# Kernel optimization log

Measured on AMD Instinct MI355X. Metric: run time of the kernel, lower is better.

## Reference

```python
import jax, jax.numpy as jnp
import numpy as np

N_NODES = 10000
N_EDGES = 320000
IN_DIM = 128
HID = 256


def setup_inputs() -> dict:
    key = jax.random.key(0)
    ks = jax.random.split(key, 10)
    s_in = 1.0 / np.sqrt(IN_DIM)
    s_h = 1.0 / np.sqrt(HID)
    return {
        "x": jax.random.normal(ks[0], (N_NODES, IN_DIM), dtype=jnp.float32),
        "edge_index": jax.random.randint(ks[1], (2, N_EDGES), 0, N_NODES, dtype=jnp.int64),
        # feature_projector Linear(IN_DIM -> HID)
        "Wp": jax.random.uniform(ks[2], (IN_DIM, HID), jnp.float32, -s_in, s_in),
        "bp": jax.random.uniform(ks[3], (HID,), jnp.float32, -s_in, s_in),
        # LSTM(input=HID, hidden=HID) params, torch layout [4H, H], gate order i,f,g,o
        "W_ih": jax.random.uniform(ks[4], (4 * HID, HID), jnp.float32, -s_h, s_h),
        "W_hh": jax.random.uniform(ks[5], (4 * HID, HID), jnp.float32, -s_h, s_h),
        "b_ih": jax.random.uniform(ks[6], (4 * HID,), jnp.float32, -s_h, s_h),
        "b_hh": jax.random.uniform(ks[7], (4 * HID,), jnp.float32, -s_h, s_h),
        # EvolveGCN-O initial weight [H, H] (glorot-style)
        "initial_weight": jax.random.normal(ks[8], (HID, HID), dtype=jnp.float32) * np.sqrt(2.0 / (2 * HID)),
        # GCNConv bias
        "b_gcn": jnp.zeros((HID,), dtype=jnp.float32),
    }


def _forward(x, edge_index, Wp, bp, W_ih, W_hh, b_ih, b_hh, initial_weight, b_gcn):
    n = x.shape[0]
    # 1) feature projection
    h = x @ Wp + bp  # [N, H]
    # 2) EvolveGCN-O: one LSTM step on the weight matrix (rows = batch),
    #    with h0 = c0 = initial_weight; evolved hidden state is the GCN weight.
    gates = initial_weight @ W_ih.T + b_ih + initial_weight @ W_hh.T + b_hh  # [H, 4H]
    i_g, f_g, g_g, o_g = jnp.split(gates, 4, axis=-1)
    c = jax.nn.sigmoid(f_g) * initial_weight + jax.nn.sigmoid(i_g) * jnp.tanh(g_g)
    W = jax.nn.sigmoid(o_g) * jnp.tanh(c)  # [H, H]
    # 3) GCN propagation with fixed W: out = D^{-1/2}(A+I)D^{-1/2} (h W) + b
    hw = h @ W  # [N, H]
    self_loop = jnp.arange(n, dtype=edge_index.dtype)
    src = jnp.concatenate([edge_index[0], self_loop])
    dst = jnp.concatenate([edge_index[1], self_loop])
    ones = jnp.ones(src.shape[0], dtype=hw.dtype)
    deg = jax.ops.segment_sum(ones, dst, num_segments=n)  # in-degree incl. self loop
    dinv = jnp.where(deg > 0, jax.lax.rsqrt(deg), 0.0)
    norm = dinv[src] * dinv[dst]  # [E+N]
    out = jax.ops.segment_sum(hw[src] * norm[:, None], dst, num_segments=n)
    return out + b_gcn


def reference(x, edge_index, Wp, bp, W_ih, W_hh, b_ih, b_hh, initial_weight, b_gcn):
    return _forward(x, edge_index, Wp, bp, W_ih, W_hh, b_ih, b_hh, initial_weight, b_gcn)
```

## Files before the change

kernel.cpp:

```cpp
#include <hip/hip_runtime.h>
#include <math.h>

#define N_NODES 10000
#define N_EDGES 320000
#define IN_DIM  128
#define HID     256
#define CAP     128

#define NB_GATES 64
#define NB_FILL  313
#define NB_XCVT  80


__device__ __forceinline__ unsigned bf16rne(float f) {
    union { float f; unsigned u; } c; c.f = f;
    return (c.u + 0x7FFFu + ((c.u >> 16) & 1u)) >> 16;
}

__global__ __launch_bounds__(256)
void k_prep(const int* __restrict__ ei, int* __restrict__ cursor,
            int* __restrict__ bucket, const float* __restrict__ iw,
            const float* __restrict__ wih, const float* __restrict__ whh,
            float* __restrict__ G, const float* __restrict__ x,
            unsigned* __restrict__ xb) {
    __shared__ float smem[8192];
    if (blockIdx.x >= NB_GATES + NB_FILL) {
        int tid = (blockIdx.x - NB_GATES - NB_FILL) * 256 + threadIdx.x;
        const float2* x2 = (const float2*)x;
        #pragma unroll
        for (int it = 0; it < 32; ++it) {
            int idx = tid + it * (NB_XCVT * 256);
            if (idx < N_NODES * 64) {
                float2 v = x2[idx];
                xb[idx] = bf16rne(v.x) | (bf16rne(v.y) << 16);
            }
        }
        return;
    }
    if (blockIdx.x >= NB_GATES) {
        int e = ((blockIdx.x - NB_GATES) * 256 + threadIdx.x) * 4;
        if (e + 3 < N_EDGES) {
            int4 s4 = *(const int4*)&ei[e];
            int4 d4 = *(const int4*)&ei[N_EDGES + e];
            int p0 = atomicAdd(&cursor[d4.x], 1);
            if (p0 < CAP) bucket[d4.x * CAP + p0] = s4.x;
            int p1 = atomicAdd(&cursor[d4.y], 1);
            if (p1 < CAP) bucket[d4.y * CAP + p1] = s4.y;
            int p2 = atomicAdd(&cursor[d4.z], 1);
            if (p2 < CAP) bucket[d4.z * CAP + p2] = s4.z;
            int p3 = atomicAdd(&cursor[d4.w], 1);
            if (p3 < CAP) bucket[d4.w * CAP + p3] = s4.w;
        } else {
            for (int q = e; q < N_EDGES; ++q) {
                int s = ei[q];
                int d = ei[N_EDGES + q];
                int pos = atomicAdd(&cursor[d], 1);
                if (pos < CAP) bucket[d * CAP + pos] = s;
            }
        }
        return;
    }
    int bid = blockIdx.x;
    int m0 = (bid & 3) * 64, n0 = (bid >> 2) * 64;
    float (*aT)[64] = (float(*)[64])smem;
    float (*bS)[64] = (float(*)[64])(smem + 4096);
    int t = threadIdx.x;
    int tm = t & 15, tn = t >> 4;
    float acc[4][4] = {};
    for (int kt = 0; kt < 4; ++kt) {
        int k0 = kt * 64;
        int row = t >> 2;
        #pragma unroll
        for (int r = 0; r < 4; ++r) {
            int k4 = 4 * (t & 3) + r;
            float4 av = *(const float4*)&iw[(m0 + row) * HID + k0 + 4 * k4];
            aT[4 * k4 + 0][row] = av.x; aT[4 * k4 + 1][row] = av.y;
            aT[4 * k4 + 2][row] = av.z; aT[4 * k4 + 3][row] = av.w;
            float4 b1 = *(const float4*)&wih[(n0 + row) * HID + k0 + 4 * k4];
            float4 b2 = *(const float4*)&whh[(n0 + row) * HID + k0 + 4 * k4];
            bS[4 * k4 + 0][row] = b1.x + b2.x; bS[4 * k4 + 1][row] = b1.y + b2.y;
            bS[4 * k4 + 2][row] = b1.z + b2.z; bS[4 * k4 + 3][row] = b1.w + b2.w;
        }
        __syncthreads();
        #pragma unroll 8
        for (int kk = 0; kk < 64; ++kk) {
            float4 a4 = *(const float4*)&aT[kk][4 * tm];
            float4 b4 = *(const float4*)&bS[kk][4 * tn];
            float a[4] = {a4.x, a4.y, a4.z, a4.w};
            float b[4] = {b4.x, b4.y, b4.z, b4.w};
            #pragma unroll
            for (int i = 0; i < 4; ++i)
                #pragma unroll
                for (int j = 0; j < 4; ++j)
                    acc[i][j] = fmaf(a[i], b[j], acc[i][j]);
        }
        __syncthreads();
    }
    #pragma unroll
    for (int i = 0; i < 4; ++i) {
        float4 o = make_float4(acc[i][0], acc[i][1], acc[i][2], acc[i][3]);
        *(float4*)&G[(m0 + 4 * tm + i) * 1024 + n0 + 4 * tn] = o;
    }
}

__global__ __launch_bounds__(256)
void k_wev_dinv(const float* __restrict__ G, const float* __restrict__ iw,
                const float* __restrict__ b_ih, const float* __restrict__ b_hh,
                float* __restrict__ Wev, const int* __restrict__ cursor,
                float* __restrict__ dinv) {
    if (blockIdx.x >= 256) {
        int v = (blockIdx.x - 256) * 256 + threadIdx.x;
        if (v < N_NODES) dinv[v] = rsqrtf((float)(cursor[v] + 1));
        return;
    }
    int r = blockIdx.x;
    int j = threadIdx.x;
    float gi = G[r * 1024 + 0   + j] + b_ih[0   + j] + b_hh[0   + j];
    float gf = G[r * 1024 + 256 + j] + b_ih[256 + j] + b_hh[256 + j];
    float gg = G[r * 1024 + 512 + j] + b_ih[512 + j] + b_hh[512 + j];
    float go = G[r * 1024 + 768 + j] + b_ih[768 + j] + b_hh[768 + j];
    float si = 1.f / (1.f + expf(-gi));
    float sf = 1.f / (1.f + expf(-gf));
    float so = 1.f / (1.f + expf(-go));
    float c  = sf * iw[r * HID + j] + si * tanhf(gg);
    Wev[r * HID + j] = so * tanhf(c);
}

__global__ __launch_bounds__(256)
void k_wc_agg(const unsigned* __restrict__ xb, const int* __restrict__ bucket,
              const int* __restrict__ cursor, const float* __restrict__ dinv,
              float* __restrict__ y, float* __restrict__ rs,
              const float* __restrict__ Wp, const float* __restrict__ bp,
              const float* __restrict__ Wev, float* __restrict__ Wc,
              float* __restrict__ bc) {
    __shared__ float arow[HID];
    if (blockIdx.x < 129) {
        int a = blockIdx.x;
        int j = threadIdx.x;
        const float* srcRow = (a < IN_DIM) ? &Wp[a * HID] : bp;
        arow[j] = srcRow[j];
        __syncthreads();
        float acc = 0.f;
        #pragma unroll 4
        for (int k = 0; k < HID; ++k)
            acc = fmaf(arow[k], Wev[k * HID + j], acc);
        if (a < IN_DIM) Wc[a * HID + j] = acc;
        else            bc[j] = acc;
        return;
    }
    int wv   = threadIdx.x >> 6;
    int lane = threadIdx.x & 63;
    int v = (blockIdx.x - 129) * 4 + wv;
    int cntv = cursor[v];
    float dv = dinv[v];
    int cnt = cntv > CAP ? CAP : cntv;
    unsigned self = xb[v * 64 + lane];
    union { unsigned u; float f; } c0, c1;
    c0.u = self << 16; c1.u = self & 0xFFFF0000u;
    float acc0 = dv * c0.f, acc1 = dv * c1.f;
    float wsum = dv;
    const int4* bkt4 = (const int4*)&bucket[v * CAP];
    int j = 0;
    for (; j + 4 <= cnt; j += 4) {
        int4 s = bkt4[j >> 2];
        float w0 = dinv[s.x], w1 = dinv[s.y], w2 = dinv[s.z], w3 = dinv[s.w];
        unsigned r0 = xb[s.x * 64 + lane];
        unsigned r1 = xb[s.y * 64 + lane];
        unsigned r2 = xb[s.z * 64 + lane];
        unsigned r3 = xb[s.w * 64 + lane];
        union { unsigned u; float f; } a0, a1;
        a0.u = r0 << 16; a1.u = r0 & 0xFFFF0000u;
        acc0 = fmaf(w0, a0.f, acc0); acc1 = fmaf(w0, a1.f, acc1);
        a0.u = r1 << 16; a1.u = r1 & 0xFFFF0000u;
        acc0 = fmaf(w1, a0.f, acc0); acc1 = fmaf(w1, a1.f, acc1);
        a0.u = r2 << 16; a1.u = r2 & 0xFFFF0000u;
        acc0 = fmaf(w2, a0.f, acc0); acc1 = fmaf(w2, a1.f, acc1);
        a0.u = r3 << 16; a1.u = r3 & 0xFFFF0000u;
        acc0 = fmaf(w3, a0.f, acc0); acc1 = fmaf(w3, a1.f, acc1);
        wsum += w0 + w1 + w2 + w3;
    }
    for (; j < cnt; ++j) {
        int s = ((const int*)bkt4)[j];
        float w = dinv[s];
        unsigned r = xb[s * 64 + lane];
        union { unsigned u; float f; } a0, a1;
        a0.u = r << 16; a1.u = r & 0xFFFF0000u;
        acc0 = fmaf(w, a0.f, acc0); acc1 = fmaf(w, a1.f, acc1);
        wsum += w;
    }
    float2 o; o.x = dv * acc0; o.y = dv * acc1;
    ((float2*)y)[v * 64 + lane] = o;
    if (lane == 0) rs[v] = dv * wsum;
}

__global__ __launch_bounds__(256)
void k_out(const float* __restrict__ y, const float* __restrict__ Wc,
           const float* __restrict__ bc, const float* __restrict__ rs,
           const float* __restrict__ b_gcn, float* __restrict__ out) {
    __shared__ float yT[64][64];
    __shared__ float wcS[64][128];
    int m0 = blockIdx.x * 64, n0 = blockIdx.y * 128;
    int t = threadIdx.x;
    int tn = t & 31, tm = t >> 5;
    float acc[8][4] = {};
    for (int kc = 0; kc < 2; ++kc) {
        {
            int m = t >> 2, kq = t & 3;
            int gm = m0 + m;
            #pragma unroll
            for (int r = 0; r < 4; ++r) {
                int kk = kq * 16 + r * 4;
                float4 v = (gm < N_NODES)
                    ? *(const float4*)&y[gm * IN_DIM + kc * 64 + kk]
                    : make_float4(0.f, 0.f, 0.f, 0.f);
                yT[kk + 0][m] = v.x; yT[kk + 1][m] = v.y;
                yT[kk + 2][m] = v.z; yT[kk + 3][m] = v.w;
            }
        }
        {
            int k = t >> 2, cq = t & 3;
            #pragma unroll
            for (int r = 0; r < 8; ++r) {
                int col = 32 * cq + 4 * r;
                *(float4*)&wcS[k][col] =
                    *(const float4*)&Wc[(kc * 64 + k) * HID + n0 + col];
            }
        }
        __syncthreads();
        #pragma unroll 4
        for (int k = 0; k < 64; ++k) {
            float4 a0 = *(const float4*)&yT[k][8 * tm];
            float4 a1 = *(const float4*)&yT[k][8 * tm + 4];
            float4 b  = *(const float4*)&wcS[k][4 * tn];
            float a[8] = {a0.x, a0.y, a0.z, a0.w, a1.x, a1.y, a1.z, a1.w};
            float bb[4] = {b.x, b.y, b.z, b.w};
            #pragma unroll
            for (int i = 0; i < 8; ++i)
                #pragma unroll
                for (int j = 0; j < 4; ++j)
                    acc[i][j] = fmaf(a[i], bb[j], acc[i][j]);
        }
        __syncthreads();
    }
    float4 bcv = *(const float4*)&bc[n0 + 4 * tn];
    float4 bg  = *(const float4*)&b_gcn[n0 + 4 * tn];
    #pragma unroll
    for (int i = 0; i < 8; ++i) {
        int mm = m0 + 8 * tm + i;
        if (mm < N_NODES) {
            float rsv = rs[mm];
            float4 o;
            o.x = acc[i][0] + rsv * bcv.x + bg.x;
            o.y = acc[i][1] + rsv * bcv.y + bg.y;
            o.z = acc[i][2] + rsv * bcv.z + bg.z;
            o.w = acc[i][3] + rsv * bcv.w + bg.w;
            *(float4*)&out[mm * HID + n0 + 4 * tn] = o;
        }
    }
}

extern "C" void kernel_launch(void* const* d_in, const int* in_sizes, int n_in,
                              void* d_out, int out_size, void* d_ws, size_t ws_size,
                              hipStream_t stream) {
    const float* x     = (const float*)d_in[0];
    const int*   ei    = (const int*)d_in[1];
    const float* Wp    = (const float*)d_in[2];
    const float* bp    = (const float*)d_in[3];
    const float* W_ih  = (const float*)d_in[4];
    const float* W_hh  = (const float*)d_in[5];
    const float* b_ih  = (const float*)d_in[6];
    const float* b_hh  = (const float*)d_in[7];
    const float* iw    = (const float*)d_in[8];
    const float* b_gcn = (const float*)d_in[9];
    float* out = (float*)d_out;

    char* ws = (char*)d_ws;
    float*    y      = (float*)   (ws + 0);
    float*    G      = (float*)   (ws + 5120000);
    float*    Wev    = (float*)   (ws + 6168576);
    float*    Wc     = (float*)   (ws + 6430720);
    float*    bc     = (float*)   (ws + 6561792);
    float*    rs     = (float*)   (ws + 6562816);
    unsigned* xb     = (unsigned*)(ws + 6602816);
    int*      cursor = (int*)     (ws + 9162816);
    float*    dinv   = (float*)   (ws + 9202816);
    int*      bucket = (int*)     (ws + 9242816);

    hipMemsetAsync(cursor, 0, N_NODES * sizeof(int), stream);

    k_prep<<<NB_GATES + NB_FILL + NB_XCVT, 256, 0, stream>>>(
        ei, cursor, bucket, iw, W_ih, W_hh, G, x, xb);
    k_wev_dinv<<<256 + 40, 256, 0, stream>>>(G, iw, b_ih, b_hh, Wev, cursor, dinv);
    k_wc_agg<<<129 + 2500, 256, 0, stream>>>(xb, bucket, cursor, dinv, y, rs, Wp, bp, Wev, Wc, bc);
    k_out<<<dim3(157, 2), 256, 0, stream>>>(y, Wc, bc, rs, b_gcn, out);
}
```

Before: 148.6 us.

## Use bf16 MFMA for output GEMM, store y and Wc in bf16, retile gates GEMM

Replaces the fp32 FMA-tiled output GEMM with a bf16 MFMA 16x16x32 kernel. The aggregated features y and the combined weight Wc (now stored transposed) are written as bf16, which halves their traffic and feeds the matrix cores directly. The gate GEMM uses smaller 32x64 tiles over twice as many blocks, and the sigmoid/tanh calls become fast __expf forms. This costs precision from bf16 rounding of y and Wc and from the approximate transcendentals.

```diff
diff --git a/kernel.cpp b/kernel.cpp
--- a/kernel.cpp
+++ b/kernel.cpp
@@ -7,9 +7,12 @@
 #define HID     256
 #define CAP     128
 
-#define NB_GATES 64
+#define NB_GATES 128
 #define NB_FILL  313
 #define NB_XCVT  80
+
+typedef __attribute__((ext_vector_type(8))) short frag_ab;
+typedef __attribute__((ext_vector_type(4))) float frag_cd;
 
 
 __device__ __forceinline__ unsigned bf16rne(float f) {
@@ -23,7 +26,7 @@
             const float* __restrict__ wih, const float* __restrict__ whh,
             float* __restrict__ G, const float* __restrict__ x,
             unsigned* __restrict__ xb) {
-    __shared__ float smem[8192];
+    __shared__ float smem[6144];
     if (blockIdx.x >= NB_GATES + NB_FILL) {
         int tid = (blockIdx.x - NB_GATES - NB_FILL) * 256 + threadIdx.x;
         const float2* x2 = (const float2*)x;
@@ -61,35 +64,44 @@
         return;
     }
     int bid = blockIdx.x;
-    int m0 = (bid & 3) * 64, n0 = (bid >> 2) * 64;
-    float (*aT)[64] = (float(*)[64])smem;
-    float (*bS)[64] = (float(*)[64])(smem + 4096);
+    int m0 = (bid & 7) * 32, n0 = (bid >> 3) * 64;
+    float (*aT)[32] = (float(*)[32])smem;
+    float (*bS)[64] = (float(*)[64])(smem + 2048);
     int t = threadIdx.x;
     int tm = t & 15, tn = t >> 4;
-    float acc[4][4] = {};
+    float acc[2][4] = {};
     for (int kt = 0; kt < 4; ++kt) {
         int k0 = kt * 64;
-        int row = t >> 2;
-        #pragma unroll
-        for (int r = 0; r < 4; ++r) {
-            int k4 = 4 * (t & 3) + r;
-            float4 av = *(const float4*)&iw[(m0 + row) * HID + k0 + 4 * k4];
-            aT[4 * k4 + 0][row] = av.x; aT[4 * k4 + 1][row] = av.y;
-            aT[4 * k4 + 2][row] = av.z; aT[4 * k4 + 3][row] = av.w;
-            float4 b1 = *(const float4*)&wih[(n0 + row) * HID + k0 + 4 * k4];
-            float4 b2 = *(const float4*)&whh[(n0 + row) * HID + k0 + 4 * k4];
-            bS[4 * k4 + 0][row] = b1.x + b2.x; bS[4 * k4 + 1][row] = b1.y + b2.y;
-            bS[4 * k4 + 2][row] = b1.z + b2.z; bS[4 * k4 + 3][row] = b1.w + b2.w;
+        {
+            int row = t >> 3;
+            #pragma unroll
+            for (int r = 0; r < 2; ++r) {
+                int kq = 2 * (t & 7) + r;
+                float4 av = *(const float4*)&iw[(m0 + row) * HID + k0 + 4 * kq];
+                aT[4 * kq + 0][row] = av.x; aT[4 * kq + 1][row] = av.y;
+                aT[4 * kq + 2][row] = av.z; aT[4 * kq + 3][row] = av.w;
+            }
+        }
+        {
+            int row = t >> 2;
+            #pragma unroll
+            for (int r = 0; r < 4; ++r) {
+                int kq = 4 * (t & 3) + r;
+                float4 b1 = *(const float4*)&wih[(n0 + row) * HID + k0 + 4 * kq];
+                float4 b2 = *(const float4*)&whh[(n0 + row) * HID + k0 + 4 * kq];
+                bS[4 * kq + 0][row] = b1.x + b2.x; bS[4 * kq + 1][row] = b1.y + b2.y;
+                bS[4 * kq + 2][row] = b1.z + b2.z; bS[4 * kq + 3][row] = b1.w + b2.w;
+            }
         }
         __syncthreads();
         #pragma unroll 8
         for (int kk = 0; kk < 64; ++kk) {
-            float4 a4 = *(const float4*)&aT[kk][4 * tm];
+            float2 a2 = *(const float2*)&aT[kk][2 * tm];
             float4 b4 = *(const float4*)&bS[kk][4 * tn];
-            float a[4] = {a4.x, a4.y, a4.z, a4.w};
+            float a[2] = {a2.x, a2.y};
             float b[4] = {b4.x, b4.y, b4.z, b4.w};
             #pragma unroll
-            for (int i = 0; i < 4; ++i)
+            for (int i = 0; i < 2; ++i)
                 #pragma unroll
                 for (int j = 0; j < 4; ++j)
                     acc[i][j] = fmaf(a[i], b[j], acc[i][j]);
@@ -97,11 +109,14 @@
         __syncthreads();
     }
     #pragma unroll
-    for (int i = 0; i < 4; ++i) {
+    for (int i = 0; i < 2; ++i) {
         float4 o = make_float4(acc[i][0], acc[i][1], acc[i][2], acc[i][3]);
-        *(float4*)&G[(m0 + 4 * tm + i) * 1024 + n0 + 4 * tn] = o;
-    }
-}
+        *(float4*)&G[(m0 + 2 * tm + i) * 1024 + n0 + 4 * tn] = o;
+    }
+}
+
+__device__ __forceinline__ float sig_f(float x)  { return 1.f / (1.f + __expf(-x)); }
+__device__ __forceinline__ float tanh_f(float x) { return 1.f - 2.f / (1.f + __expf(2.f * x)); }
 
 __global__ __launch_bounds__(256)
 void k_wev_dinv(const float* __restrict__ G, const float* __restrict__ iw,
@@ -119,19 +134,16 @@
     float gf = G[r * 1024 + 256 + j] + b_ih[256 + j] + b_hh[256 + j];
     float gg = G[r * 1024 + 512 + j] + b_ih[512 + j] + b_hh[512 + j];
     float go = G[r * 1024 + 768 + j] + b_ih[768 + j] + b_hh[768 + j];
-    float si = 1.f / (1.f + expf(-gi));
-    float sf = 1.f / (1.f + expf(-gf));
-    float so = 1.f / (1.f + expf(-go));
-    float c  = sf * iw[r * HID + j] + si * tanhf(gg);
-    Wev[r * HID + j] = so * tanhf(c);
+    float c  = sig_f(gf) * iw[r * HID + j] + sig_f(gi) * tanh_f(gg);
+    Wev[r * HID + j] = sig_f(go) * tanh_f(c);
 }
 
 __global__ __launch_bounds__(256)
 void k_wc_agg(const unsigned* __restrict__ xb, const int* __restrict__ bucket,
               const int* __restrict__ cursor, const float* __restrict__ dinv,
-              float* __restrict__ y, float* __restrict__ rs,
+              unsigned* __restrict__ yb, float* __restrict__ rs,
               const float* __restrict__ Wp, const float* __restrict__ bp,
-              const float* __restrict__ Wev, float* __restrict__ Wc,
+              const float* __restrict__ Wev, unsigned* __restrict__ wct,
               float* __restrict__ bc) {
     __shared__ float arow[HID];
     if (blockIdx.x < 129) {
@@ -144,8 +156,10 @@
         #pragma unroll 4
         for (int k = 0; k < HID; ++k)
             acc = fmaf(arow[k], Wev[k * HID + j], acc);
-        if (a < IN_DIM) Wc[a * HID + j] = acc;
-        else            bc[j] = acc;
+        if (a < IN_DIM)
+            ((unsigned short*)wct)[j * IN_DIM + a] = (unsigned short)bf16rne(acc);
+        else
+            bc[j] = acc;
         return;
     }
     int wv   = threadIdx.x >> 6;
@@ -188,73 +202,43 @@
         acc0 = fmaf(w, a0.f, acc0); acc1 = fmaf(w, a1.f, acc1);
         wsum += w;
     }
-    float2 o; o.x = dv * acc0; o.y = dv * acc1;
-    ((float2*)y)[v * 64 + lane] = o;
+    yb[v * 64 + lane] = bf16rne(dv * acc0) | (bf16rne(dv * acc1) << 16);
     if (lane == 0) rs[v] = dv * wsum;
 }
 
 __global__ __launch_bounds__(256)
-void k_out(const float* __restrict__ y, const float* __restrict__ Wc,
+void k_out(const unsigned* __restrict__ yb, const unsigned* __restrict__ wct,
            const float* __restrict__ bc, const float* __restrict__ rs,
            const float* __restrict__ b_gcn, float* __restrict__ out) {
-    __shared__ float yT[64][64];
-    __shared__ float wcS[64][128];
-    int m0 = blockIdx.x * 64, n0 = blockIdx.y * 128;
-    int t = threadIdx.x;
-    int tn = t & 31, tm = t >> 5;
-    float acc[8][4] = {};
-    for (int kc = 0; kc < 2; ++kc) {
-        {
-            int m = t >> 2, kq = t & 3;
-            int gm = m0 + m;
-            #pragma unroll
-            for (int r = 0; r < 4; ++r) {
-                int kk = kq * 16 + r * 4;
-                float4 v = (gm < N_NODES)
-                    ? *(const float4*)&y[gm * IN_DIM + kc * 64 + kk]
-                    : make_float4(0.f, 0.f, 0.f, 0.f);
-                yT[kk + 0][m] = v.x; yT[kk + 1][m] = v.y;
-                yT[kk + 2][m] = v.z; yT[kk + 3][m] = v.w;
-            }
-        }
-        {
-            int k = t >> 2, cq = t & 3;
-            #pragma unroll
-            for (int r = 0; r < 8; ++r) {
-                int col = 32 * cq + 4 * r;
-                *(float4*)&wcS[k][col] =
-                    *(const float4*)&Wc[(kc * 64 + k) * HID + n0 + col];
-            }
-        }
-        __syncthreads();
-        #pragma unroll 4
-        for (int k = 0; k < 64; ++k) {
-            float4 a0 = *(const float4*)&yT[k][8 * tm];
-            float4 a1 = *(const float4*)&yT[k][8 * tm + 4];
-            float4 b  = *(const float4*)&wcS[k][4 * tn];
-            float a[8] = {a0.x, a0.y, a0.z, a0.w, a1.x, a1.y, a1.z, a1.w};
-            float bb[4] = {b.x, b.y, b.z, b.w};
-            #pragma unroll
-            for (int i = 0; i < 8; ++i)
-                #pragma unroll
-                for (int j = 0; j < 4; ++j)
-                    acc[i][j] = fmaf(a[i], bb[j], acc[i][j]);
-        }
-        __syncthreads();
-    }
-    float4 bcv = *(const float4*)&bc[n0 + 4 * tn];
-    float4 bg  = *(const float4*)&b_gcn[n0 + 4 * tn];
-    #pragma unroll
-    for (int i = 0; i < 8; ++i) {
-        int mm = m0 + 8 * tm + i;
-        if (mm < N_NODES) {
-            float rsv = rs[mm];
-            float4 o;
-            o.x = acc[i][0] + rsv * bcv.x + bg.x;
-            o.y = acc[i][1] + rsv * bcv.y + bg.y;
-            o.z = acc[i][2] + rsv * bcv.z + bg.z;
-            o.w = acc[i][3] + rsv * bcv.w + bg.w;
-            *(float4*)&out[mm * HID + n0 + 4 * tn] = o;
+    int m0 = blockIdx.x * 16;
+    int w = threadIdx.x >> 6, lane = threadIdx.x & 63;
+    int q = lane >> 4, ln = lane & 15;
+    const int4* yb4  = (const int4*)yb;
+    const int4* wct4 = (const int4*)wct;
+    union { int4 v; frag_ab f; } a[4];
+    #pragma unroll
+    for (int kc = 0; kc < 4; ++kc)
+        a[kc].v = yb4[(m0 + ln) * 16 + kc * 4 + q];
+    float rsv[4];
+    #pragma unroll
+    for (int r = 0; r < 4; ++r) rsv[r] = rs[m0 + q * 4 + r];
+    #pragma unroll
+    for (int i = 0; i < 4; ++i) {
+        int n0 = (w + 4 * i) * 16;
+        union { int4 v; frag_ab f; } b[4];
+        #pragma unroll
+        for (int kc = 0; kc < 4; ++kc)
+            b[kc].v = wct4[(n0 + ln) * 16 + kc * 4 + q];
+        frag_cd acc = {0.f, 0.f, 0.f, 0.f};
+        #pragma unroll
+        for (int kc = 0; kc < 4; ++kc)
+            acc = __builtin_amdgcn_mfma_f32_16x16x32_bf16(a[kc].f, b[kc].f, acc, 0, 0, 0);
+        int n = n0 + ln;
+        float bcv = bc[n], bgv = b_gcn[n];
+        #pragma unroll
+        for (int r = 0; r < 4; ++r) {
+            int m = m0 + q * 4 + r;
+            out[m * HID + n] = acc[r] + rsv[r] * bcv + bgv;
         }
     }
 }
@@ -275,22 +259,22 @@
     float* out = (float*)d_out;
 
     char* ws = (char*)d_ws;
-    float*    y      = (float*)   (ws + 0);
-    float*    G      = (float*)   (ws + 5120000);
-    float*    Wev    = (float*)   (ws + 6168576);
-    float*    Wc     = (float*)   (ws + 6430720);
-    float*    bc     = (float*)   (ws + 6561792);
-    float*    rs     = (float*)   (ws + 6562816);
-    unsigned* xb     = (unsigned*)(ws + 6602816);
-    int*      cursor = (int*)     (ws + 9162816);
-    float*    dinv   = (float*)   (ws + 9202816);
-    int*      bucket = (int*)     (ws + 9242816);
+    unsigned* yb     = (unsigned*)(ws + 0);
+    float*    G      = (float*)   (ws + 2560000);
+    float*    Wev    = (float*)   (ws + 3608576);
+    unsigned* wct    = (unsigned*)(ws + 3870720);
+    float*    bc     = (float*)   (ws + 3936256);
+    float*    rs     = (float*)   (ws + 3937280);
+    unsigned* xb     = (unsigned*)(ws + 3977280);
+    int*      cursor = (int*)     (ws + 6537280);
+    float*    dinv   = (float*)   (ws + 6577280);
+    int*      bucket = (int*)     (ws + 6617280);
 
     hipMemsetAsync(cursor, 0, N_NODES * sizeof(int), stream);
 
     k_prep<<<NB_GATES + NB_FILL + NB_XCVT, 256, 0, stream>>>(
         ei, cursor, bucket, iw, W_ih, W_hh, G, x, xb);
     k_wev_dinv<<<256 + 40, 256, 0, stream>>>(G, iw, b_ih, b_hh, Wev, cursor, dinv);
-    k_wc_agg<<<129 + 2500, 256, 0, stream>>>(xb, bucket, cursor, dinv, y, rs, Wp, bp, Wev, Wc, bc);
-    k_out<<<dim3(157, 2), 256, 0, stream>>>(y, Wc, bc, rs, b_gcn, out);
-}
+    k_wc_agg<<<129 + 2500, 256, 0, stream>>>(xb, bucket, cursor, dinv, yb, rs, Wp, bp, Wev, wct, bc);
+    k_out<<<625, 256, 0, stream>>>(yb, wct, bc, rs, b_gcn, out);
+}
```

After: 136.5 us. 1.09x faster.
